# Kernel tuning notes

Hardware: AMD Instinct MI355X
Metric: run time of the kernel (lower is better)

Reference implementation:

```python
import jax, jax.numpy as jnp
import numpy as np

B, D = 32768, 512
DEPTH = 7
ORDERS = (1, 2, 3, 5)
COUPLING_STRENGTH = 1.0


def _damping_coeffs():
    # frequency_dependent profile: 0.1 / (1 + exp(linspace(0, 3, D)))
    freqs = jnp.exp(jnp.linspace(0.0, 3.0, D))
    return 0.1 / (1.0 + freqs)


def _generate_harmonics(wave, hmats):
    acc = jnp.zeros_like(wave)
    for order, H in zip(ORDERS, hmats):
        hw = wave @ H.astype(wave.dtype)
        if order == 1:
            h = hw
        elif order == 2:
            h = hw * jnp.conj(hw)
        elif order == 3:
            h = hw * jnp.conj(hw) * hw
        else:
            mag = jnp.abs(hw)
            ph = jnp.angle(hw)
            h = (mag ** (1.0 / order)) * jnp.exp(1j * (ph * float(order)))
        acc = acc + h * (1.0 / (order * order))
    return acc


def _nonlinearity(wave, scale, bias):
    re = jnp.tanh(wave.real * scale + bias)
    im = jnp.tanh(wave.imag * scale + bias)
    return jax.lax.complex(re, im)


def _forward(wave_real, wave_imag, coupling_matrix, harmonic_1, harmonic_2,
             harmonic_3, harmonic_5, mixing_scale, mixing_bias):
    wave = jax.lax.complex(wave_real, wave_imag)  # [B, D] complex64
    hmats = (harmonic_1, harmonic_2, harmonic_3, harmonic_5)
    damping = _damping_coeffs()  # [D], non-trainable constant

    chamber = wave
    history = []
    for depth in range(DEPTH):
        transformed = (chamber @ coupling_matrix.astype(chamber.dtype)) * COUPLING_STRENGTH
        with_harmonics = transformed + _generate_harmonics(chamber, hmats)
        if depth > 0:
            # InterferenceLayer approximated as complex wave superposition
            interference = chamber + with_harmonics
        else:
            interference = with_harmonics
        nl = _nonlinearity(interference, mixing_scale, mixing_bias)
        factor = jnp.exp(-damping * float(depth)).astype(jnp.float32)
        chamber = nl * factor.astype(nl.dtype)
        history.append(chamber)

    w = jnp.exp(-jnp.linspace(0.0, 2.0, DEPTH))
    w = w / jnp.sum(w)
    stacked = jnp.stack(history)  # [DEPTH, B, D]
    out = jnp.sum(stacked * w[:, None, None].astype(stacked.dtype), axis=0)
    return out


def setup_inputs() -> dict:
    key = jax.random.key(0)
    ks = jax.random.split(key, 8)
    s = 1.0 / np.sqrt(D)  # approx orthogonal init scale
    return {
        "wave_real": jax.random.normal(ks[0], (B, D), jnp.float32),
        "wave_imag": jax.random.normal(ks[1], (B, D), jnp.float32),
        "coupling_matrix": jax.random.normal(ks[2], (D, D), jnp.float32) * s,
        "harmonic_1": jax.random.normal(ks[3], (D, D), jnp.float32) * s,
        "harmonic_2": jax.random.normal(ks[4], (D, D), jnp.float32) * s,
        "harmonic_3": jax.random.normal(ks[5], (D, D), jnp.float32) * s,
        "harmonic_5": jax.random.normal(ks[6], (D, D), jnp.float32) * s,
        "mixing_scale": jnp.ones((D,), jnp.float32),
        "mixing_bias": jnp.zeros((D,), jnp.float32),
    }


def reference(wave_real, wave_imag, coupling_matrix, harmonic_1, harmonic_2,
              harmonic_3, harmonic_5, mixing_scale, mixing_bias):
    out = _forward(wave_real, wave_imag, coupling_matrix, harmonic_1,
                   harmonic_2, harmonic_3, harmonic_5, mixing_scale, mixing_bias)
    # return as stacked real/imag float32 [2, B, D] for harness comparability
    return jnp.stack([out.real, out.imag])
```

## Files before the change

### kernel.cpp

```cpp
#include <hip/hip_runtime.h>
#include <hip/hip_bf16.h>
#include <cstdint>


typedef __bf16 bf16_t;
typedef bf16_t bf16x8 __attribute__((ext_vector_type(8)));
typedef float f32x4 __attribute__((ext_vector_type(4)));
typedef _Float16 h2_t __attribute__((ext_vector_type(2)));

#define B_ROWS 32768
#define D_DIM 512
#define N_DEPTH 7
#define CROWS 16
#define MAT_SZ (32 * 16 * 64 * 8)
#define HI_SZ (4 * MAT_SZ)

__device__ __forceinline__ unsigned short f2b(float f) {
  bf16_t h = (bf16_t)f;
  return __builtin_bit_cast(unsigned short, h);
}
__device__ __forceinline__ float b2f(unsigned short u) {
  bf16_t h = __builtin_bit_cast(bf16_t, u);
  return (float)h;
}
__device__ __forceinline__ float fast_tanh(float x) {
  float ax = fabsf(x);
  float e = __expf(2.0f * ax);
  float t = 1.0f - 2.0f / (e + 1.0f);
  return copysignf(t, x);
}

__global__ __launch_bounds__(256) void prepack_kernel(
    const float* __restrict__ cm, const float* __restrict__ h1,
    const float* __restrict__ h2, const float* __restrict__ h3,
    const float* __restrict__ h5, unsigned short* __restrict__ dst) {
  int gid = blockIdx.x * 256 + threadIdx.x;
  if (gid >= 4 * 32 * 16 * 64) return;
  int l  = gid & 63;
  int ks = (gid >> 6) & 15;
  int t  = (gid >> 10) & 31;
  int o  = gid >> 15;
  int n  = t * 16 + (l & 15);
  int k0 = ks * 32 + (l >> 4) * 8;
  unsigned short* ph = dst + (size_t)gid * 8;
  int lop = (o == 0) ? 0 : (o == 3) ? 1 : -1;
  unsigned short* pl = (lop >= 0)
      ? dst + HI_SZ + (size_t)lop * MAT_SZ + (size_t)(gid & 32767) * 8
      : nullptr;
#pragma unroll
  for (int i = 0; i < 8; ++i) {
    size_t idx = (size_t)(k0 + i) * D_DIM + n;
    float v = (o == 0) ? (cm[idx] + h1[idx])
            : (o == 1) ? h2[idx]
            : (o == 2) ? h3[idx]
                       : h5[idx];
    unsigned short h = f2b(v);
    ph[i] = h;
    if (pl) pl[i] = f2b(v - b2f(h));
  }
}

__device__ __forceinline__ int lds_addr(int row, int byte_in_row) {
  return row * 1024 + (byte_in_row ^ ((row & 7) << 4));
}

__global__ __launch_bounds__(512) void resonance_kernel(
    const float* __restrict__ wr, const float* __restrict__ wi,
    const float* __restrict__ scale, const float* __restrict__ bias,
    const unsigned short* __restrict__ pre, float* __restrict__ out) {
  __shared__ unsigned short lds_hi[32 * 512];
  __shared__ unsigned short lds_lo[32 * 512];

  const int tid  = threadIdx.x;
  const int lane = tid & 63;
  const int wave = tid >> 6;
  const int ln15 = lane & 15;
  const int lg   = lane >> 4;
  const int r0   = blockIdx.x * CROWS;

#pragma unroll
  for (int it = 0; it < 4; ++it) {
    int idx = it * 512 + tid;
    int row = idx >> 6;
    int k0  = (idx & 63) * 8;
    const float* src = (row < CROWS)
        ? (wr + (size_t)(r0 + row) * D_DIM + k0)
        : (wi + (size_t)(r0 + row - CROWS) * D_DIM + k0);
    float4 v0 = *(const float4*)(src);
    float4 v1 = *(const float4*)(src + 4);
    float v[8] = {v0.x, v0.y, v0.z, v0.w, v1.x, v1.y, v1.z, v1.w};
    bf16x8 ph, pl;
#pragma unroll
    for (int j = 0; j < 8; ++j) {
      unsigned short h = f2b(v[j]);
      ph[j] = __builtin_bit_cast(bf16_t, h);
      pl[j] = (bf16_t)(v[j] - b2f(h));
    }
    int ad = lds_addr(row, k0 * 2);
    *(bf16x8*)((char*)lds_hi + ad) = ph;
    *(bf16x8*)((char*)lds_lo + ad) = pl;
  }
  __syncthreads();

  float Wsum = 0.0f;
#pragma unroll
  for (int d = 0; d < N_DEPTH; ++d) Wsum += __expf(-(float)d * (1.0f / 3.0f));
  const float invW = 1.0f / Wsum;

  h2_t oacc[4][4];
  h2_t news[4][4];
#pragma unroll
  for (int c = 0; c < 4; ++c)
#pragma unroll
    for (int r = 0; r < 4; ++r) oacc[c][r] = (h2_t){(_Float16)0.f, (_Float16)0.f};

  for (int depth = 0; depth < N_DEPTH; ++depth) {
    const float wd = __expf(-(float)depth * (1.0f / 3.0f)) * invW;

#pragma unroll
    for (int c = 0; c < 4; ++c) {
      const int t = c * 8 + wave;
      f32x4 acc0[2], acc1[2], acc2[2], acc3[2];
#pragma unroll
      for (int mt = 0; mt < 2; ++mt) {
        acc0[mt] = (f32x4){0.f, 0.f, 0.f, 0.f};
        acc1[mt] = (f32x4){0.f, 0.f, 0.f, 0.f};
        acc2[mt] = (f32x4){0.f, 0.f, 0.f, 0.f};
        acc3[mt] = (f32x4){0.f, 0.f, 0.f, 0.f};
      }

#pragma unroll 2
      for (int ks = 0; ks < 16; ++ks) {
        bf16x8 ah[2], al[2];
#pragma unroll
        for (int mt = 0; mt < 2; ++mt) {
          int ad = lds_addr(mt * 16 + ln15, ks * 64 + lg * 16);
          ah[mt] = *(const bf16x8*)((const char*)lds_hi + ad);
          al[mt] = *(const bf16x8*)((const char*)lds_lo + ad);
        }
        const unsigned short* bb = pre + (size_t)(t * 16 + ks) * 512 + lane * 8;
        bf16x8 b0h = *(const bf16x8*)(bb);
        bf16x8 b1h = *(const bf16x8*)(bb + 1 * MAT_SZ);
        bf16x8 b2h = *(const bf16x8*)(bb + 2 * MAT_SZ);
        bf16x8 b3h = *(const bf16x8*)(bb + 3 * MAT_SZ);
        bf16x8 b0l = *(const bf16x8*)(bb + HI_SZ);
        bf16x8 b3l = *(const bf16x8*)(bb + HI_SZ + MAT_SZ);
#pragma unroll
        for (int mt = 0; mt < 2; ++mt) {
          acc0[mt] = __builtin_amdgcn_mfma_f32_16x16x32_bf16(ah[mt], b0h, acc0[mt], 0, 0, 0);
          acc0[mt] = __builtin_amdgcn_mfma_f32_16x16x32_bf16(al[mt], b0h, acc0[mt], 0, 0, 0);
          acc0[mt] = __builtin_amdgcn_mfma_f32_16x16x32_bf16(ah[mt], b0l, acc0[mt], 0, 0, 0);
          acc1[mt] = __builtin_amdgcn_mfma_f32_16x16x32_bf16(ah[mt], b1h, acc1[mt], 0, 0, 0);
          acc2[mt] = __builtin_amdgcn_mfma_f32_16x16x32_bf16(ah[mt], b2h, acc2[mt], 0, 0, 0);
          acc3[mt] = __builtin_amdgcn_mfma_f32_16x16x32_bf16(ah[mt], b3h, acc3[mt], 0, 0, 0);
          acc3[mt] = __builtin_amdgcn_mfma_f32_16x16x32_bf16(al[mt], b3h, acc3[mt], 0, 0, 0);
          acc3[mt] = __builtin_amdgcn_mfma_f32_16x16x32_bf16(ah[mt], b3l, acc3[mt], 0, 0, 0);
        }
      }

      const int col = t * 16 + ln15;
      const float sclv = scale[col];
      const float biav = bias[col];
      const float damp = 0.1f / (1.0f + __expf(3.0f * (float)col * (1.0f / 511.0f)));
      const float fac  = __expf(-damp * (float)depth);
#pragma unroll
      for (int r = 0; r < 4; ++r) {
        float lr = acc0[0][r],  li = acc0[1][r];
        float re2 = acc1[0][r], im2 = acc1[1][r];
        float ar = 0.25f * (re2 * re2 + im2 * im2);
        float re3 = acc2[0][r], im3 = acc2[1][r];
        float m3 = re3 * re3 + im3 * im3;
        ar += 0.111111111f * m3 * re3;
        float ai = 0.111111111f * m3 * im3;
        float re5 = acc3[0][r], im5 = acc3[1][r];
        float m5 = re5 * re5 + im5 * im5;
        {
          float m5c = fmaxf(m5, 1e-36f);
          float inv = rsqrtf(m5c);
          float ur = re5 * inv, ui = im5 * inv;
          float u2r = ur * ur - ui * ui,     u2i = 2.0f * ur * ui;
          float u4r = u2r * u2r - u2i * u2i, u4i = 2.0f * u2r * u2i;
          float u5r = u4r * ur - u4i * ui,   u5i = u4r * ui + u4i * ur;
          float mag = __expf(0.1f * __logf(m5c));
          float msk = (m5 > 1e-36f) ? 0.04f : 0.0f;
          ar += msk * mag * u5r;
          ai += msk * mag * u5i;
        }
        float ir = lr + ar, ii = li + ai;
        if (depth > 0) {
          ir += (float)news[c][r][0];
          ii += (float)news[c][r][1];
        }
        float cre = fast_tanh(ir * sclv + biav) * fac;
        float cim = fast_tanh(ii * sclv + biav) * fac;
        oacc[c][r] += (h2_t){(_Float16)(wd * cre), (_Float16)(wd * cim)};
        news[c][r] = (h2_t){(_Float16)cre, (_Float16)cim};
      }
    }

    if (depth < N_DEPTH - 1) {
      __syncthreads();
#pragma unroll
      for (int c = 0; c < 4; ++c) {
        const int colb = ((c * 8 + wave) * 16 + ln15) * 2;
#pragma unroll
        for (int r = 0; r < 4; ++r) {
          const int brow = lg * 4 + r;
          float cre = (float)news[c][r][0];
          float cim = (float)news[c][r][1];
          unsigned short hr = f2b(cre);
          unsigned short lr = f2b(cre - b2f(hr));
          unsigned short hi = f2b(cim);
          unsigned short li = f2b(cim - b2f(hi));
          int ar_ = lds_addr(brow, colb);
          int ai_ = lds_addr(brow + CROWS, colb);
          *(unsigned short*)((char*)lds_hi + ar_) = hr;
          *(unsigned short*)((char*)lds_lo + ar_) = lr;
          *(unsigned short*)((char*)lds_hi + ai_) = hi;
          *(unsigned short*)((char*)lds_lo + ai_) = li;
        }
      }
      __syncthreads();
    }
  }

#pragma unroll
  for (int c = 0; c < 4; ++c) {
    const int col = (c * 8 + wave) * 16 + ln15;
#pragma unroll
    for (int r = 0; r < 4; ++r) {
      int brow = lg * 4 + r;
      size_t base = (size_t)(r0 + brow) * D_DIM + col;
      out[base] = (float)oacc[c][r][0];
      out[(size_t)B_ROWS * D_DIM + base] = (float)oacc[c][r][1];
    }
  }
}

extern "C" void kernel_launch(void* const* d_in, const int* in_sizes, int n_in,
                              void* d_out, int out_size, void* d_ws, size_t ws_size,
                              hipStream_t stream) {
  const float* wr = (const float*)d_in[0];
  const float* wi = (const float*)d_in[1];
  const float* cm = (const float*)d_in[2];
  const float* h1 = (const float*)d_in[3];
  const float* h2 = (const float*)d_in[4];
  const float* h3 = (const float*)d_in[5];
  const float* h5 = (const float*)d_in[6];
  const float* sc = (const float*)d_in[7];
  const float* bi = (const float*)d_in[8];
  unsigned short* pre = (unsigned short*)d_ws;
  float* out = (float*)d_out;

  hipLaunchKernelGGL(prepack_kernel, dim3(512), dim3(256), 0, stream,
                     cm, h1, h2, h3, h5, pre);
  hipLaunchKernelGGL(resonance_kernel, dim3(B_ROWS / CROWS), dim3(512), 0, stream,
                     wr, wi, sc, bi, pre, out);
}
```

Baseline: 2.088 ms.

## Split fused depth loop into per-depth kernel launches with global state

The single persistent kernel, which held the running output and state in registers across all 7 depths, is replaced by 7 launches of a per-depth kernel. Each launch reads the previous chamber state (bf16 hi/lo pairs) from workspace, does the matmul and epilogue, then writes the new state and accumulates the output in global memory. The weight prepack is also interleaved so that each k-step's six B fragments sit next to each other. The aim is to drop the register pressure from the per-depth accumulators and to raise occupancy (waves_per_eu 4). The cost is extra global traffic for the state and output on every depth, plus launch overhead. The old path is kept as a fallback when the workspace is too small.

```diff
diff --git a/kernel.cpp b/kernel.cpp
--- a/kernel.cpp
+++ b/kernel.cpp
@@ -1,6 +1,7 @@
 #include <hip/hip_runtime.h>
 #include <hip/hip_bf16.h>
 #include <cstdint>
+#include <math.h>
 
 
 typedef __bf16 bf16_t;
@@ -11,7 +12,11 @@
 #define B_ROWS 32768
 #define D_DIM 512
 #define N_DEPTH 7
-#define CROWS 16
+#define BD ((size_t)B_ROWS * D_DIM)
+
+#define STATE_OFF ((size_t)4 << 20)
+#define WS_NEED (STATE_OFF + BD * 8)
+
 #define MAT_SZ (32 * 16 * 64 * 8)
 #define HI_SZ (4 * MAT_SZ)
 
@@ -29,8 +34,204 @@
   float t = 1.0f - 2.0f / (e + 1.0f);
   return copysignf(t, x);
 }
-
-__global__ __launch_bounds__(256) void prepack_kernel(
+__device__ __forceinline__ int lds_addr(int row, int byte_in_row) {
+  return row * 1024 + (byte_in_row ^ ((row & 7) << 4));
+}
+
+
+__global__ __launch_bounds__(256) void prepack_v2(
+    const float* __restrict__ cm, const float* __restrict__ h1,
+    const float* __restrict__ h2, const float* __restrict__ h3,
+    const float* __restrict__ h5, unsigned short* __restrict__ dst) {
+  int gid = blockIdx.x * 256 + threadIdx.x;
+  if (gid >= 32 * 16 * 64) return;
+  int l  = gid & 63;
+  int ks = (gid >> 6) & 15;
+  int t  = gid >> 10;
+  int n  = t * 16 + (l & 15);
+  int k0 = ks * 32 + (l >> 4) * 8;
+  unsigned short* base = dst + ((size_t)(t * 16 + ks) * 6) * 512 + l * 8;
+  bf16x8 f0, f1, f2, f3, f4, f5;
+#pragma unroll
+  for (int i = 0; i < 8; ++i) {
+    size_t idx = (size_t)(k0 + i) * D_DIM + n;
+    float v0 = cm[idx] + h1[idx];
+    unsigned short h0 = f2b(v0);
+    f0[i] = __builtin_bit_cast(bf16_t, h0);
+    f1[i] = (bf16_t)(v0 - b2f(h0));
+    f2[i] = (bf16_t)h2[idx];
+    f3[i] = (bf16_t)h3[idx];
+    float v5 = h5[idx];
+    unsigned short h5v = f2b(v5);
+    f4[i] = __builtin_bit_cast(bf16_t, h5v);
+    f5[i] = (bf16_t)(v5 - b2f(h5v));
+  }
+  *(bf16x8*)(base + 0 * 512) = f0;
+  *(bf16x8*)(base + 1 * 512) = f1;
+  *(bf16x8*)(base + 2 * 512) = f2;
+  *(bf16x8*)(base + 3 * 512) = f3;
+  *(bf16x8*)(base + 4 * 512) = f4;
+  *(bf16x8*)(base + 5 * 512) = f5;
+}
+
+__global__ __launch_bounds__(512) __attribute__((amdgpu_waves_per_eu(4)))
+void depth_kernel(
+    const float* __restrict__ wr, const float* __restrict__ wi,
+    const float* __restrict__ scale, const float* __restrict__ bias,
+    const unsigned short* __restrict__ pre, uint32_t* __restrict__ state,
+    float* __restrict__ out, int depth, float wd) {
+  __shared__ unsigned short lds_hi[32 * 512];
+  __shared__ unsigned short lds_lo[32 * 512];
+
+  const int tid  = threadIdx.x;
+  const int lane = tid & 63;
+  const int wave = tid >> 6;
+  const int ln15 = lane & 15;
+  const int lg   = lane >> 4;
+  const int r0   = blockIdx.x * 16;
+
+  if (depth == 0) {
+#pragma unroll
+    for (int it = 0; it < 4; ++it) {
+      int idx = it * 512 + tid;
+      int row = idx >> 6;
+      int k0  = (idx & 63) * 8;
+      const float* src = (row < 16)
+          ? (wr + (size_t)(r0 + row) * D_DIM + k0)
+          : (wi + (size_t)(r0 + row - 16) * D_DIM + k0);
+      float4 v0 = *(const float4*)(src);
+      float4 v1 = *(const float4*)(src + 4);
+      float v[8] = {v0.x, v0.y, v0.z, v0.w, v1.x, v1.y, v1.z, v1.w};
+      bf16x8 ph, pl;
+#pragma unroll
+      for (int j = 0; j < 8; ++j) {
+        unsigned short h = f2b(v[j]);
+        ph[j] = __builtin_bit_cast(bf16_t, h);
+        pl[j] = (bf16_t)(v[j] - b2f(h));
+      }
+      int ad = lds_addr(row, k0 * 2);
+      *(bf16x8*)((char*)lds_hi + ad) = ph;
+      *(bf16x8*)((char*)lds_lo + ad) = pl;
+    }
+  } else {
+#pragma unroll
+    for (int it = 0; it < 8; ++it) {
+      int idx = it * 512 + tid;
+      int row = idx >> 8;
+      int c0  = (idx & 255) * 2;
+      const uint4 v = *(const uint4*)(state + ((size_t)(r0 + row) * D_DIM + c0) * 2);
+      uint32_t hre = (v.x & 0xffffu) | ((v.z & 0xffffu) << 16);
+      uint32_t lre = (v.x >> 16)     | (v.z & 0xffff0000u);
+      uint32_t him = (v.y & 0xffffu) | ((v.w & 0xffffu) << 16);
+      uint32_t lim = (v.y >> 16)     | (v.w & 0xffff0000u);
+      int adr = lds_addr(row, c0 * 2);
+      int adi = lds_addr(row + 16, c0 * 2);
+      *(uint32_t*)((char*)lds_hi + adr) = hre;
+      *(uint32_t*)((char*)lds_lo + adr) = lre;
+      *(uint32_t*)((char*)lds_hi + adi) = him;
+      *(uint32_t*)((char*)lds_lo + adi) = lim;
+    }
+  }
+  __syncthreads();
+
+#pragma unroll
+  for (int c = 0; c < 4; ++c) {
+    const int t = c * 8 + wave;
+    f32x4 acc0[2], acc1[2], acc2[2], acc3[2];
+#pragma unroll
+    for (int mt = 0; mt < 2; ++mt) {
+      acc0[mt] = (f32x4){0.f, 0.f, 0.f, 0.f};
+      acc1[mt] = (f32x4){0.f, 0.f, 0.f, 0.f};
+      acc2[mt] = (f32x4){0.f, 0.f, 0.f, 0.f};
+      acc3[mt] = (f32x4){0.f, 0.f, 0.f, 0.f};
+    }
+
+    const unsigned short* bb = pre + ((size_t)(t * 16) * 6 + 3) * 512 + lane * 8;
+#pragma unroll 2
+    for (int ks = 0; ks < 16; ++ks) {
+      bf16x8 ah[2], al[2];
+#pragma unroll
+      for (int mt = 0; mt < 2; ++mt) {
+        int ad = lds_addr(mt * 16 + ln15, ks * 64 + lg * 16);
+        ah[mt] = *(const bf16x8*)((const char*)lds_hi + ad);
+        al[mt] = *(const bf16x8*)((const char*)lds_lo + ad);
+      }
+      bf16x8 b0h = *(const bf16x8*)(bb - 1536);
+      bf16x8 b0l = *(const bf16x8*)(bb - 1024);
+      bf16x8 b1h = *(const bf16x8*)(bb - 512);
+      bf16x8 b2h = *(const bf16x8*)(bb);
+      bf16x8 b3h = *(const bf16x8*)(bb + 512);
+      bf16x8 b3l = *(const bf16x8*)(bb + 1024);
+      bb += 3072;
+#pragma unroll
+      for (int mt = 0; mt < 2; ++mt) {
+        acc0[mt] = __builtin_amdgcn_mfma_f32_16x16x32_bf16(ah[mt], b0h, acc0[mt], 0, 0, 0);
+        acc0[mt] = __builtin_amdgcn_mfma_f32_16x16x32_bf16(al[mt], b0h, acc0[mt], 0, 0, 0);
+        acc0[mt] = __builtin_amdgcn_mfma_f32_16x16x32_bf16(ah[mt], b0l, acc0[mt], 0, 0, 0);
+        acc1[mt] = __builtin_amdgcn_mfma_f32_16x16x32_bf16(ah[mt], b1h, acc1[mt], 0, 0, 0);
+        acc2[mt] = __builtin_amdgcn_mfma_f32_16x16x32_bf16(ah[mt], b2h, acc2[mt], 0, 0, 0);
+        acc3[mt] = __builtin_amdgcn_mfma_f32_16x16x32_bf16(ah[mt], b3h, acc3[mt], 0, 0, 0);
+        acc3[mt] = __builtin_amdgcn_mfma_f32_16x16x32_bf16(al[mt], b3h, acc3[mt], 0, 0, 0);
+        acc3[mt] = __builtin_amdgcn_mfma_f32_16x16x32_bf16(ah[mt], b3l, acc3[mt], 0, 0, 0);
+      }
+    }
+
+    const int col = t * 16 + ln15;
+    const float sclv = scale[col];
+    const float biav = bias[col];
+    const float damp = 0.1f / (1.0f + __expf(3.0f * (float)col * (1.0f / 511.0f)));
+    const float fac  = __expf(-damp * (float)depth);
+#pragma unroll
+    for (int r = 0; r < 4; ++r) {
+      const int brow = lg * 4 + r;
+      float lr = acc0[0][r],  li = acc0[1][r];
+      float re2 = acc1[0][r], im2 = acc1[1][r];
+      float ar = 0.25f * (re2 * re2 + im2 * im2);
+      float re3 = acc2[0][r], im3 = acc2[1][r];
+      float m3 = re3 * re3 + im3 * im3;
+      ar += 0.111111111f * m3 * re3;
+      float ai = 0.111111111f * m3 * im3;
+      float re5 = acc3[0][r], im5 = acc3[1][r];
+      float m5 = re5 * re5 + im5 * im5;
+      {
+        float m5c = fmaxf(m5, 1e-36f);
+        float inv = rsqrtf(m5c);
+        float ur = re5 * inv, ui = im5 * inv;
+        float u2r = ur * ur - ui * ui,     u2i = 2.0f * ur * ui;
+        float u4r = u2r * u2r - u2i * u2i, u4i = 2.0f * u2r * u2i;
+        float u5r = u4r * ur - u4i * ui,   u5i = u4r * ui + u4i * ur;
+        float mag = __expf(0.1f * __logf(m5c));
+        float msk = (m5 > 1e-36f) ? 0.04f : 0.0f;
+        ar += msk * mag * u5r;
+        ai += msk * mag * u5i;
+      }
+      float ir = lr + ar, ii = li + ai;
+      size_t base = (size_t)(r0 + brow) * D_DIM + col;
+      if (depth > 0) {
+        int cb = col * 2;
+        ir += b2f(*(const unsigned short*)((const char*)lds_hi + lds_addr(brow, cb)))
+            + b2f(*(const unsigned short*)((const char*)lds_lo + lds_addr(brow, cb)));
+        ii += b2f(*(const unsigned short*)((const char*)lds_hi + lds_addr(brow + 16, cb)))
+            + b2f(*(const unsigned short*)((const char*)lds_lo + lds_addr(brow + 16, cb)));
+      }
+      float cre = fast_tanh(ir * sclv + biav) * fac;
+      float cim = fast_tanh(ii * sclv + biav) * fac;
+      unsigned short hr = f2b(cre);
+      unsigned short hi = f2b(cim);
+      uint2 sv;
+      sv.x = (uint32_t)hr | ((uint32_t)f2b(cre - b2f(hr)) << 16);
+      sv.y = (uint32_t)hi | ((uint32_t)f2b(cim - b2f(hi)) << 16);
+      *(uint2*)(state + base * 2) = sv;
+      float ore = wd * cre, oim = wd * cim;
+      if (depth > 0) { ore += out[base]; oim += out[BD + base]; }
+      out[base] = ore;
+      out[BD + base] = oim;
+    }
+  }
+}
+
+
+__global__ __launch_bounds__(256) void prepack_r6(
     const float* __restrict__ cm, const float* __restrict__ h1,
     const float* __restrict__ h2, const float* __restrict__ h3,
     const float* __restrict__ h5, unsigned short* __restrict__ dst) {
@@ -60,32 +261,26 @@
   }
 }
 
-__device__ __forceinline__ int lds_addr(int row, int byte_in_row) {
-  return row * 1024 + (byte_in_row ^ ((row & 7) << 4));
-}
-
 __global__ __launch_bounds__(512) void resonance_kernel(
     const float* __restrict__ wr, const float* __restrict__ wi,
     const float* __restrict__ scale, const float* __restrict__ bias,
     const unsigned short* __restrict__ pre, float* __restrict__ out) {
   __shared__ unsigned short lds_hi[32 * 512];
   __shared__ unsigned short lds_lo[32 * 512];
-
   const int tid  = threadIdx.x;
   const int lane = tid & 63;
   const int wave = tid >> 6;
   const int ln15 = lane & 15;
   const int lg   = lane >> 4;
-  const int r0   = blockIdx.x * CROWS;
-
+  const int r0   = blockIdx.x * 16;
 #pragma unroll
   for (int it = 0; it < 4; ++it) {
     int idx = it * 512 + tid;
     int row = idx >> 6;
     int k0  = (idx & 63) * 8;
-    const float* src = (row < CROWS)
+    const float* src = (row < 16)
         ? (wr + (size_t)(r0 + row) * D_DIM + k0)
-        : (wi + (size_t)(r0 + row - CROWS) * D_DIM + k0);
+        : (wi + (size_t)(r0 + row - 16) * D_DIM + k0);
     float4 v0 = *(const float4*)(src);
     float4 v1 = *(const float4*)(src + 4);
     float v[8] = {v0.x, v0.y, v0.z, v0.w, v1.x, v1.y, v1.z, v1.w};
@@ -101,22 +296,18 @@
     *(bf16x8*)((char*)lds_lo + ad) = pl;
   }
   __syncthreads();
-
   float Wsum = 0.0f;
 #pragma unroll
   for (int d = 0; d < N_DEPTH; ++d) Wsum += __expf(-(float)d * (1.0f / 3.0f));
   const float invW = 1.0f / Wsum;
-
   h2_t oacc[4][4];
   h2_t news[4][4];
 #pragma unroll
   for (int c = 0; c < 4; ++c)
 #pragma unroll
     for (int r = 0; r < 4; ++r) oacc[c][r] = (h2_t){(_Float16)0.f, (_Float16)0.f};
-
   for (int depth = 0; depth < N_DEPTH; ++depth) {
     const float wd = __expf(-(float)depth * (1.0f / 3.0f)) * invW;
-
 #pragma unroll
     for (int c = 0; c < 4; ++c) {
       const int t = c * 8 + wave;
@@ -128,7 +319,6 @@
         acc2[mt] = (f32x4){0.f, 0.f, 0.f, 0.f};
         acc3[mt] = (f32x4){0.f, 0.f, 0.f, 0.f};
       }
-
 #pragma unroll 2
       for (int ks = 0; ks < 16; ++ks) {
         bf16x8 ah[2], al[2];
@@ -157,7 +347,6 @@
           acc3[mt] = __builtin_amdgcn_mfma_f32_16x16x32_bf16(ah[mt], b3l, acc3[mt], 0, 0, 0);
         }
       }
-
       const int col = t * 16 + ln15;
       const float sclv = scale[col];
       const float biav = bias[col];
@@ -197,7 +386,6 @@
         news[c][r] = (h2_t){(_Float16)cre, (_Float16)cim};
       }
     }
-
     if (depth < N_DEPTH - 1) {
       __syncthreads();
 #pragma unroll
@@ -213,7 +401,7 @@
           unsigned short hi = f2b(cim);
           unsigned short li = f2b(cim - b2f(hi));
           int ar_ = lds_addr(brow, colb);
-          int ai_ = lds_addr(brow + CROWS, colb);
+          int ai_ = lds_addr(brow + 16, colb);
           *(unsigned short*)((char*)lds_hi + ar_) = hr;
           *(unsigned short*)((char*)lds_lo + ar_) = lr;
           *(unsigned short*)((char*)lds_hi + ai_) = hi;
@@ -223,7 +411,6 @@
       __syncthreads();
     }
   }
-
 #pragma unroll
   for (int c = 0; c < 4; ++c) {
     const int col = (c * 8 + wave) * 16 + ln15;
@@ -232,10 +419,11 @@
       int brow = lg * 4 + r;
       size_t base = (size_t)(r0 + brow) * D_DIM + col;
       out[base] = (float)oacc[c][r][0];
-      out[(size_t)B_ROWS * D_DIM + base] = (float)oacc[c][r][1];
-    }
-  }
-}
+      out[BD + base] = (float)oacc[c][r][1];
+    }
+  }
+}
+
 
 extern "C" void kernel_launch(void* const* d_in, const int* in_sizes, int n_in,
                               void* d_out, int out_size, void* d_ws, size_t ws_size,
@@ -249,11 +437,25 @@
   const float* h5 = (const float*)d_in[6];
   const float* sc = (const float*)d_in[7];
   const float* bi = (const float*)d_in[8];
-  unsigned short* pre = (unsigned short*)d_ws;
   float* out = (float*)d_out;
 
-  hipLaunchKernelGGL(prepack_kernel, dim3(512), dim3(256), 0, stream,
-                     cm, h1, h2, h3, h5, pre);
-  hipLaunchKernelGGL(resonance_kernel, dim3(B_ROWS / CROWS), dim3(512), 0, stream,
-                     wr, wi, sc, bi, pre, out);
-}
+  if (ws_size >= WS_NEED) {
+    unsigned short* pre = (unsigned short*)d_ws;
+    uint32_t* state = (uint32_t*)((char*)d_ws + STATE_OFF);
+    hipLaunchKernelGGL(prepack_v2, dim3(128), dim3(256), 0, stream,
+                       cm, h1, h2, h3, h5, pre);
+    double Wsum = 0.0;
+    for (int d = 0; d < N_DEPTH; ++d) Wsum += exp(-(double)d / 3.0);
+    for (int d = 0; d < N_DEPTH; ++d) {
+      float wd = (float)(exp(-(double)d / 3.0) / Wsum);
+      hipLaunchKernelGGL(depth_kernel, dim3(B_ROWS / 16), dim3(512), 0, stream,
+                         wr, wi, sc, bi, pre, state, out, d, wd);
+    }
+  } else {
+    unsigned short* pre = (unsigned short*)d_ws;
+    hipLaunchKernelGGL(prepack_r6, dim3(512), dim3(256), 0, stream,
+                       cm, h1, h2, h3, h5, pre);
+    hipLaunchKernelGGL(resonance_kernel, dim3(B_ROWS / 16), dim3(512), 0, stream,
+                       wr, wi, sc, bi, pre, out);
+  }
+}
```

After: 2.324 ms. 11.3% more time.
